# Optimization experiments

Measured on AMD Instinct MI355X. Metric: run time of the kernel, lower is better.

Reference implementation:

```python
import jax, jax.numpy as jnp
import numpy as np

NUM_HEADS = 8
SCALE = 3
TOPKS = [16, 8, 8]  # index 0 = coarsest level


def avg_pool2(t):
    B, C, H, W = t.shape
    return t.reshape(B, C, H // 2, 2, W // 2, 2).mean(axis=(3, 5))


def _to_heads(t, Hi, Wi):
    # [B, C, Hi, Wi] with C = nh*hd (head-major channels) -> [B, nh, Hi*Wi, hd]
    B, C = t.shape[0], t.shape[1]
    hd = C // NUM_HEADS
    return t.reshape(B, NUM_HEADS, hd, Hi * Wi).transpose(0, 1, 3, 2)


def setup_inputs() -> dict:
    key = jax.random.key(0)
    ks = jax.random.split(key, 6)
    B, H, W, C = 2, 96, 96, 128
    N = H * W
    s = 0.02
    return {
        "x": jax.random.normal(ks[0], (B, N, C), jnp.float32),
        "target": jax.random.normal(ks[1], (B, N, C), jnp.float32),
        "Wq": jax.random.normal(ks[2], (C, C), jnp.float32) * s,
        "Wk": jax.random.normal(ks[3], (C, C), jnp.float32) * s,
        "Wv": jax.random.normal(ks[4], (C, C), jnp.float32) * s,
        "Wo": jax.random.normal(ks[5], (C, C), jnp.float32) * s,
        "bo": jnp.zeros((C,), jnp.float32),
        "H": 96,
        "W": 96,
    }


def reference(x, target, Wq, Wk, Wv, Wo, bo, H, W):
    B, N, C = x.shape
    hd = C // NUM_HEADS
    temp = 1.0 / jnp.sqrt(jnp.float32(hd))
    xi = x.transpose(0, 2, 1).reshape(B, C, H, W)
    ti = target.transpose(0, 2, 1).reshape(B, C, H, W)
    # 1x1 conv projections == channel-wise matmul
    q = jnp.einsum('bchw,oc->bohw', xi, Wq)
    k = jnp.einsum('bchw,oc->bohw', ti, Wk)
    v = jnp.einsum('bchw,oc->bohw', ti, Wv)
    qs, ks_, vs, hw = [], [], [], []
    for i in range(SCALE):
        Hi, Wi = H >> i, W >> i
        qs.append(_to_heads(q, Hi, Wi))
        ks_.append(_to_heads(k, Hi, Wi))
        vs.append(_to_heads(v, Hi, Wi))
        hw.append((Hi, Wi))
        if i != SCALE - 1:
            q, k, v = avg_pool2(q), avg_pool2(k), avg_pool2(v)
    # ---- coarsest level: full attention + top-k key selection ----
    i = SCALE - 1
    A = jax.nn.softmax(temp * jnp.einsum('bhnd,bhmd->bhnm', qs[i], ks_[i]), axis=-1)
    msg = jnp.einsum('bhnm,bhmd->bhnd', A, vs[i])  # [B,h,Nc,hd]
    topk_score, topk_idx = jax.lax.top_k(A, TOPKS[0])  # [B,h,Nc,K]
    # ---- refine coarse -> fine over quadtree children of top-k keys ----
    gather = jax.vmap(jax.vmap(lambda arr, idx: arr[idx]))  # over B, h
    for lvl in range(SCALE - 2, -1, -1):
        Hi, Wi = hw[lvl]
        Hp, Wpar = hw[lvl + 1]
        Nf = Hi * Wi
        K = topk_idx.shape[-1]
        yf, xf = jnp.divmod(jnp.arange(Nf), Wi)
        parent = (yf // 2) * Wpar + (xf // 2)  # [Nf] parent query index
        p_idx = topk_idx[:, :, parent, :]  # [B,h,Nf,K] selected coarse keys
        ky, kx = jnp.divmod(p_idx, Wpar)
        dy = jnp.array([0, 0, 1, 1], jnp.int32)
        dx = jnp.array([0, 1, 0, 1], jnp.int32)
        child = ((2 * ky)[..., None] + dy) * Wi + (2 * kx)[..., None] + dx
        cand = child.reshape(B, NUM_HEADS, Nf, K * 4)  # candidate fine keys
        kg = gather(ks_[lvl], cand)  # [B,h,Nf,4K,hd]
        vg = gather(vs[lvl], cand)
        sc = temp * jnp.einsum('bhnd,bhnkd->bhnk', qs[lvl], kg)
        Af = jax.nn.softmax(sc, axis=-1)
        msg_f = jnp.einsum('bhnk,bhnkd->bhnd', Af, vg)
        msg = msg[:, :, parent, :] + msg_f  # assemble with upsampled coarse msg
        if lvl > 0:
            kk = TOPKS[SCALE - 1 - lvl]
            ts, tp = jax.lax.top_k(Af, kk)
            topk_idx = jnp.take_along_axis(cand, tp, axis=-1)
            topk_score = ts
    out = msg.transpose(0, 2, 1, 3).reshape(B, N, C)  # head-major channels
    return out @ Wo.T + bo
```

## Files before the change

kernel.cpp:

```cpp
#include <hip/hip_runtime.h>

#define NB   2
#define NHD  8
#define BH   16
#define HD   16
#define N0   9216
#define N1   2304
#define N2   576
#define W0_  96
#define W1_  48
#define W2_  24
#define M_TOT 18432
#define TEMP 0.25f

__global__ __launch_bounds__(256) void k_proj(const float* __restrict__ x, const float* __restrict__ tg,
    const float* __restrict__ Wq, const float* __restrict__ Wk, const float* __restrict__ Wv,
    float* __restrict__ q0, float* __restrict__ k0, float* __restrict__ v0)
{
    __shared__ __align__(16) float At[16][68];
    __shared__ __align__(16) float Wt[16][132];
    const int t = threadIdx.x;
    const int which = blockIdx.y;
    const float* A  = (which==0)? x : tg;
    const float* Wm = (which==0)? Wq : (which==1? Wk : Wv);
    float* dst      = (which==0)? q0 : (which==1? k0 : v0);
    const int m0 = blockIdx.x * 64;
    const int tx = t & 15, ty = t >> 4;

    float acc[4][8];
#pragma unroll
    for(int i=0;i<4;i++)
#pragma unroll
        for(int j=0;j<8;j++) acc[i][j]=0.f;

    const int ar = t>>2, akq = (t&3)*4;
    const int wo = t>>1, wkq = (t&1)*8;

    for(int kc=0;kc<128;kc+=16){
        float4 av = *(const float4*)(A + (m0+ar)*128 + kc + akq);
        At[akq+0][ar] = av.x;
        At[akq+1][ar] = av.y;
        At[akq+2][ar] = av.z;
        At[akq+3][ar] = av.w;
        float4 w0 = *(const float4*)(Wm + wo*128 + kc + wkq);
        float4 w1 = *(const float4*)(Wm + wo*128 + kc + wkq + 4);
        Wt[wkq+0][wo] = w0.x; Wt[wkq+1][wo] = w0.y;
        Wt[wkq+2][wo] = w0.z; Wt[wkq+3][wo] = w0.w;
        Wt[wkq+4][wo] = w1.x; Wt[wkq+5][wo] = w1.y;
        Wt[wkq+6][wo] = w1.z; Wt[wkq+7][wo] = w1.w;
        __syncthreads();
#pragma unroll
        for(int kk=0;kk<16;kk++){
            float4 a4 = *(const float4*)&At[kk][ty*4];
            float4 wa = *(const float4*)&Wt[kk][tx*4];
            float4 wb = *(const float4*)&Wt[kk][64 + tx*4];
            float avr[4] = {a4.x,a4.y,a4.z,a4.w};
            float wvr[8] = {wa.x,wa.y,wa.z,wa.w, wb.x,wb.y,wb.z,wb.w};
#pragma unroll
            for(int i=0;i<4;i++)
#pragma unroll
                for(int j=0;j<8;j++) acc[i][j] += avr[i]*wvr[j];
        }
        __syncthreads();
    }
    const int hA = tx>>2, dA = (tx&3)*4;
#pragma unroll
    for(int i=0;i<4;i++){
        int m = m0 + ty*4 + i;
        int b = m / N0; int n = m - b*N0;
        float4 sA = make_float4(acc[i][0], acc[i][1], acc[i][2], acc[i][3]);
        float4 sB = make_float4(acc[i][4], acc[i][5], acc[i][6], acc[i][7]);
        *(float4*)(dst + ((b*NHD + hA    )*N0 + n)*16 + dA) = sA;
        *(float4*)(dst + ((b*NHD + hA + 4)*N0 + n)*16 + dA) = sB;
    }
}

__global__ __launch_bounds__(256) void k_pool01(const float4* __restrict__ src0,
    float4* __restrict__ dst1, float4* __restrict__ q2f,
    float4* __restrict__ k2T, float4* __restrict__ v2T)
{
    int tid = blockIdx.x*256 + threadIdx.x;
    if (tid >= 110592) return;
    int d4 = tid & 3;
    int rest = tid >> 2;
    int n2 = rest % N2; int g = rest / N2;
    int yo2 = n2 / W2_, xo2 = n2 - yo2*W2_;

    const float4* s = src0 + g*N0*4;
    float4* d1 = dst1 + g*N1*4;
    float4 l1[4];
#pragma unroll
    for(int yy=0;yy<2;yy++){
#pragma unroll
        for(int xx=0;xx<2;xx++){
            int y1 = 2*yo2+yy, x1 = 2*xo2+xx;
            int n1 = y1*W1_ + x1;
            int cbase = (2*y1)*W0_ + 2*x1;
            float4 a = s[(cbase       )*4 + d4];
            float4 b = s[(cbase+1     )*4 + d4];
            float4 c = s[(cbase+W0_   )*4 + d4];
            float4 d = s[(cbase+W0_+1 )*4 + d4];
            float4 o;
            o.x = 0.25f*(a.x+b.x+c.x+d.x);
            o.y = 0.25f*(a.y+b.y+c.y+d.y);
            o.z = 0.25f*(a.z+b.z+c.z+d.z);
            o.w = 0.25f*(a.w+b.w+c.w+d.w);
            d1[n1*4 + d4] = o;
            l1[yy*2+xx] = o;
        }
    }
    float4 o2;
    o2.x = 0.25f*(l1[0].x+l1[1].x+l1[2].x+l1[3].x);
    o2.y = 0.25f*(l1[0].y+l1[1].y+l1[2].y+l1[3].y);
    o2.z = 0.25f*(l1[0].z+l1[1].z+l1[2].z+l1[3].z);
    o2.w = 0.25f*(l1[0].w+l1[1].w+l1[2].w+l1[3].w);
    int grp = g >> 4, bh = g & 15;
    if (grp == 0)      q2f[(bh*N2 + n2)*4 + d4] = o2;
    else if (grp == 1) k2T[(bh*4 + d4)*N2 + n2] = o2;
    else               v2T[(bh*4 + d4)*N2 + n2] = o2;
}

__device__ __forceinline__ void top16_sel(const float ev[9], int lane, float* cv, int* cx, int* ip)
{
    float head = ev[0];
#pragma unroll
    for(int i=1;i<9;i++) head = fmaxf(head, ev[i]);

    float bv = head;
#pragma unroll
    for(int k=2;k<=64;k<<=1){
#pragma unroll
        for(int j=k>>1;j>=1;j>>=1){
            float pv = __shfl_xor(bv, j);
            bool keepmin = (((lane & k)==0) == ((lane & j)==0));
            bv = keepmin ? fminf(bv,pv) : fmaxf(bv,pv);
        }
    }
    float T = __shfl(bv, 48);

    int ci = 0;
#pragma unroll
    for(int i=0;i<9;i++) ci += (ev[i] >= T) ? 1 : 0;
    int ps = ci;
#pragma unroll
    for(int d=1;d<64;d<<=1){
        int t = __shfl_up(ps, d);
        if (lane >= d) ps += t;
    }
    int excl = ps - ci;
    int C = __shfl(ps, 63);

    int o = excl;
#pragma unroll
    for(int i=0;i<9;i++){
        if (ev[i] >= T){
            cv[o] = ev[i];
            cx[o] = i*64 + lane;
            o++;
        }
    }
    if (lane < 4){ cv[C+lane] = -1.0f; cx[C+lane] = 0x7fffffff; }

    for(int l=lane; l<C; l+=64){
        float mv = cv[l]; int mi = cx[l];
        int rank = 0;
        for(int c=0;c<C;c+=4){
            float4 vv = *(const float4*)(cv + c);
            int4   ii = *(const int4*)(cx + c);
            rank += (vv.x > mv || (vv.x == mv && ii.x < mi)) ? 1 : 0;
            rank += (vv.y > mv || (vv.y == mv && ii.y < mi)) ? 1 : 0;
            rank += (vv.z > mv || (vv.z == mv && ii.z < mi)) ? 1 : 0;
            rank += (vv.w > mv || (vv.w == mv && ii.w < mi)) ? 1 : 0;
        }
        if (rank < 16) ip[rank] = mi;
    }
}

__global__ __launch_bounds__(256) void k_attn2(const float* __restrict__ q2, const float* __restrict__ k2,
    const float* __restrict__ v2, float* __restrict__ msg2, int* __restrict__ idx2)
{
    __shared__ __align__(16) float cval[4][580];
    __shared__ __align__(16) int   cidx[4][580];
    const int bh = blockIdx.x;
    const int wv = threadIdx.x>>6, lane = threadIdx.x&63;
    const int qA = blockIdx.y*8 + wv*2;
    const int qB = qA + 1;

    float qrA[16], qrB[16];
    {
        const float4* qpA = (const float4*)(q2 + (bh*N2 + qA)*16);
        const float4* qpB = (const float4*)(q2 + (bh*N2 + qB)*16);
#pragma unroll
        for(int dq=0;dq<4;dq++){
            float4 va = qpA[dq];
            qrA[dq*4+0]=va.x; qrA[dq*4+1]=va.y; qrA[dq*4+2]=va.z; qrA[dq*4+3]=va.w;
            float4 vb = qpB[dq];
            qrB[dq*4+0]=vb.x; qrB[dq*4+1]=vb.y; qrB[dq*4+2]=vb.z; qrB[dq*4+3]=vb.w;
        }
    }

    const float4* kT = (const float4*)k2 + bh*4*N2;
    const float4* vT = (const float4*)v2 + bh*4*N2;

    float evA[9], evB[9];
    float mxA = -1e30f, mxB = -1e30f;
#pragma unroll
    for(int t9=0;t9<9;t9++){
        int m = t9*64 + lane;
        float sA = 0.f, sB = 0.f;
#pragma unroll
        for(int dg=0;dg<4;dg++){
            float4 kv = kT[dg*N2 + m];
            sA += qrA[dg*4+0]*kv.x + qrA[dg*4+1]*kv.y + qrA[dg*4+2]*kv.z + qrA[dg*4+3]*kv.w;
            sB += qrB[dg*4+0]*kv.x + qrB[dg*4+1]*kv.y + qrB[dg*4+2]*kv.z + qrB[dg*4+3]*kv.w;
        }
        sA *= TEMP; sB *= TEMP;
        evA[t9]=sA; evB[t9]=sB;
        mxA = fmaxf(mxA, sA);
        mxB = fmaxf(mxB, sB);
    }
#pragma unroll
    for(int st=1; st<64; st<<=1){
        mxA = fmaxf(mxA, __shfl_xor(mxA, st));
        mxB = fmaxf(mxB, __shfl_xor(mxB, st));
    }

    float sumA=0.f, sumB=0.f;
    float accA[16], accB[16];
#pragma unroll
    for(int d=0;d<16;d++){ accA[d]=0.f; accB[d]=0.f; }
#pragma unroll
    for(int t9=0;t9<9;t9++){
        int m = t9*64 + lane;
        float eA = expf(evA[t9]-mxA);
        float eB = expf(evB[t9]-mxB);
        evA[t9]=eA; evB[t9]=eB;
        sumA += eA; sumB += eB;
#pragma unroll
        for(int dg=0;dg<4;dg++){
            float4 vv = vT[dg*N2 + m];
            accA[dg*4+0] += eA*vv.x; accA[dg*4+1] += eA*vv.y;
            accA[dg*4+2] += eA*vv.z; accA[dg*4+3] += eA*vv.w;
            accB[dg*4+0] += eB*vv.x; accB[dg*4+1] += eB*vv.y;
            accB[dg*4+2] += eB*vv.z; accB[dg*4+3] += eB*vv.w;
        }
    }
#pragma unroll
    for(int st=1; st<64; st<<=1){
        sumA += __shfl_xor(sumA, st);
        sumB += __shfl_xor(sumB, st);
    }

    const bool b5 = (lane & 32) != 0;
    const bool b4 = (lane & 16) != 0;
    const bool b3 = (lane & 8) != 0;
    const bool b2 = (lane & 4) != 0;
#pragma unroll
    for(int which=0; which<2; which++){
        float* acc = which ? accB : accA;
        float sum  = which ? sumB : sumA;
        int   q    = which ? qB   : qA;
        float r8[8];
#pragma unroll
        for(int i=0;i<8;i++){
            float snd  = b5 ? acc[i]   : acc[i+8];
            float kept = b5 ? acc[i+8] : acc[i];
            r8[i] = kept + __shfl_xor(snd, 32);
        }
        float r4[4];
#pragma unroll
        for(int i=0;i<4;i++){
            float snd  = b4 ? r8[i]   : r8[i+4];
            float kept = b4 ? r8[i+4] : r8[i];
            r4[i] = kept + __shfl_xor(snd, 16);
        }
        float r2[2];
#pragma unroll
        for(int i=0;i<2;i++){
            float snd  = b3 ? r4[i]   : r4[i+2];
            float kept = b3 ? r4[i+2] : r4[i];
            r2[i] = kept + __shfl_xor(snd, 8);
        }
        {
            float snd  = b2 ? r2[0] : r2[1];
            float kept = b2 ? r2[1] : r2[0];
            r2[0] = kept + __shfl_xor(snd, 4);
        }
        r2[0] += __shfl_xor(r2[0], 2);
        r2[0] += __shfl_xor(r2[0], 1);
        float inv = 1.0f/sum;
        if ((lane&3)==0){
            msg2[(bh*N2+q)*16 + (lane>>2)] = r2[0]*inv;
        }
    }

    top16_sel(evA, lane, cval[wv], cidx[wv], idx2 + (bh*N2+qA)*16);
    top16_sel(evB, lane, cval[wv], cidx[wv], idx2 + (bh*N2+qB)*16);
}

__global__ __launch_bounds__(256) void k_ref10(
    const float* __restrict__ q1, const float* __restrict__ k1, const float* __restrict__ v1,
    const float* __restrict__ q0, const float* __restrict__ k0, const float* __restrict__ v0,
    const float* __restrict__ msg2, const int* __restrict__ idx2, float* __restrict__ msg0)
{
    __shared__ float msg1s[4][16];
    __shared__ int   idx1s[4][8];
    const int bid = (blockIdx.x & 7)*1152 + (blockIdx.x >> 3);
    const int bh = bid / 576, tile = bid - bh*576;
    const int tyy = tile / 24, txx = tile - tyy*24;
    const int py0 = tyy*2, px0 = txx*2;
    const int wv = threadIdx.x>>6, lane = threadIdx.x&63;

    const int ppy = py0 + (wv>>1), ppx = px0 + (wv&1);

    {
        const int n  = ppy*W1_ + ppx;
        const int par = (ppy>>1)*W2_ + (ppx>>1);
        const int kk = lane>>2, tt = lane&3, dy = tt>>1, dx = tt&1;
        int p = idx2[(bh*N2+par)*16 + kk];
        int ky = p / W2_, kx = p - ky*W2_;
        int child = (2*ky+dy)*W1_ + 2*kx+dx;

        const float* qp = q1 + (bh*N1+n)*16;
        float qr[16];
#pragma unroll
        for(int d=0; d<16; d+=4){
            float4 qq = *(const float4*)(qp+d);
            qr[d]=qq.x; qr[d+1]=qq.y; qr[d+2]=qq.z; qr[d+3]=qq.w;
        }
        const float4* kp = (const float4*)(k1 + (bh*N1+child)*16);
        float s = 0.f;
#pragma unroll
        for(int dq=0;dq<4;dq++){
            float4 kv = kp[dq];
            s += qr[dq*4+0]*kv.x + qr[dq*4+1]*kv.y + qr[dq*4+2]*kv.z + qr[dq*4+3]*kv.w;
        }
        s *= TEMP;
        float e = expf(s);
        float sum = e;
#pragma unroll
        for(int st=1; st<64; st<<=1) sum += __shfl_xor(sum, st);

        float acc[16];
        const float4* vp = (const float4*)(v1 + (bh*N1+child)*16);
#pragma unroll
        for(int dq=0;dq<4;dq++){
            float4 vv = vp[dq];
            acc[dq*4+0]=e*vv.x; acc[dq*4+1]=e*vv.y; acc[dq*4+2]=e*vv.z; acc[dq*4+3]=e*vv.w;
        }
        const bool b5 = (lane & 32) != 0;
        float r8[8];
#pragma unroll
        for(int ii=0;ii<8;ii++){
            float snd  = b5 ? acc[ii]   : acc[ii+8];
            float kept = b5 ? acc[ii+8] : acc[ii];
            r8[ii] = kept + __shfl_xor(snd, 32);
        }
        const bool b4 = (lane & 16) != 0;
        float r4[4];
#pragma unroll
        for(int ii=0;ii<4;ii++){
            float snd  = b4 ? r8[ii]   : r8[ii+4];
            float kept = b4 ? r8[ii+4] : r8[ii];
            r4[ii] = kept + __shfl_xor(snd, 16);
        }
        const bool b3 = (lane & 8) != 0;
        float r2[2];
#pragma unroll
        for(int ii=0;ii<2;ii++){
            float snd  = b3 ? r4[ii]   : r4[ii+2];
            float kept = b3 ? r4[ii+2] : r4[ii];
            r2[ii] = kept + __shfl_xor(snd, 8);
        }
        const bool b2 = (lane & 4) != 0;
        {
            float snd  = b2 ? r2[0] : r2[1];
            float kept = b2 ? r2[1] : r2[0];
            r2[0] = kept + __shfl_xor(snd, 4);
        }
        r2[0] += __shfl_xor(r2[0], 2);
        r2[0] += __shfl_xor(r2[0], 1);

        float inv1 = 1.0f/sum;
        if ((lane&3)==0){
            int d = lane>>2;
            msg1s[wv][d] = msg2[(bh*N2+par)*16 + d] + r2[0]*inv1;
        }

        float bv = s;
#pragma unroll
        for(int kb=2;kb<=64;kb<<=1){
#pragma unroll
            for(int jb=kb>>1;jb>=1;jb>>=1){
                float pv = __shfl_xor(bv, jb);
                bool keepmin = (((lane & kb)==0) == ((lane & jb)==0));
                bv = keepmin ? fminf(bv,pv) : fmaxf(bv,pv);
            }
        }
        float T8 = __shfl(bv, 56);
        unsigned long long mgt = __ballot(s > T8);
        unsigned long long meq = __ballot(s == T8);
        int ngt = (int)__popcll(mgt);
        int ltg = __builtin_amdgcn_mbcnt_lo((unsigned)mgt, 0);
        ltg = __builtin_amdgcn_mbcnt_hi((unsigned)(mgt>>32), ltg);
        int lte = __builtin_amdgcn_mbcnt_lo((unsigned)meq, 0);
        lte = __builtin_amdgcn_mbcnt_hi((unsigned)(meq>>32), lte);
        int slot = (s > T8) ? ltg : ((s == T8) ? (ngt + lte) : 8);
        if (slot < 8) idx1s[wv][slot] = child;
    }

    const int j = lane & 31, sub = lane >> 5;
    const int kk = j>>2, tt = j&3, dy = tt>>1, dx = tt&1;
    int p = idx1s[wv][kk];
    int ky = p / W1_, kx = p - ky*W1_;
    int child = (2*ky+dy)*W0_ + 2*kx+dx;

    float kr[16];
    {
        const float4* kp = (const float4*)(k0 + (bh*N0+child)*16);
#pragma unroll
        for(int dq=0;dq<4;dq++){
            float4 kv = kp[dq];
            kr[dq*4+0]=kv.x; kr[dq*4+1]=kv.y; kr[dq*4+2]=kv.z; kr[dq*4+3]=kv.w;
        }
    }
    const int cy0 = 2*ppy, cx0 = 2*ppx + sub;
    int nq[2];
    float s_[2];
#pragma unroll
    for(int it=0; it<2; it++){
        nq[it] = (cy0+it)*W0_ + cx0;
        const float* qp = q0 + (bh*N0+nq[it])*16;
        float qr[16];
#pragma unroll
        for(int d=0; d<16; d+=4){
            float4 qq = *(const float4*)(qp+d);
            qr[d]=qq.x; qr[d+1]=qq.y; qr[d+2]=qq.z; qr[d+3]=qq.w;
        }
        float s = 0.f;
#pragma unroll
        for(int dq=0;dq<4;dq++){
            s += qr[dq*4+0]*kr[dq*4+0] + qr[dq*4+1]*kr[dq*4+1]
               + qr[dq*4+2]*kr[dq*4+2] + qr[dq*4+3]*kr[dq*4+3];
        }
        s_[it] = s * TEMP;
    }
    float vr[16];
    {
        const float4* vp = (const float4*)(v0 + (bh*N0+child)*16);
#pragma unroll
        for(int dq=0;dq<4;dq++){
            float4 vv = vp[dq];
            vr[dq*4+0]=vv.x; vr[dq*4+1]=vv.y; vr[dq*4+2]=vv.z; vr[dq*4+3]=vv.w;
        }
    }
    const float m1d = msg1s[wv][j>>1];

#pragma unroll
    for(int it=0; it<2; it++){
        float e = expf(s_[it]);
        float sum = e;
#pragma unroll
        for(int st=1; st<32; st<<=1) sum += __shfl_xor(sum, st);

        float acc[16];
#pragma unroll
        for(int d=0;d<16;d++) acc[d] = e*vr[d];

        const bool b4 = (j & 16) != 0;
        float r8[8];
#pragma unroll
        for(int ii=0;ii<8;ii++){
            float snd  = b4 ? acc[ii]   : acc[ii+8];
            float kept = b4 ? acc[ii+8] : acc[ii];
            r8[ii] = kept + __shfl_xor(snd, 16);
        }
        const bool b3 = (j & 8) != 0;
        float r4[4];
#pragma unroll
        for(int ii=0;ii<4;ii++){
            float snd  = b3 ? r8[ii]   : r8[ii+4];
            float kept = b3 ? r8[ii+4] : r8[ii];
            r4[ii] = kept + __shfl_xor(snd, 8);
        }
        const bool b2 = (j & 4) != 0;
        float r2[2];
#pragma unroll
        for(int ii=0;ii<2;ii++){
            float snd  = b2 ? r4[ii]   : r4[ii+2];
            float kept = b2 ? r4[ii+2] : r4[ii];
            r2[ii] = kept + __shfl_xor(snd, 4);
        }
        const bool b1 = (j & 2) != 0;
        {
            float snd  = b1 ? r2[0] : r2[1];
            float kept = b1 ? r2[1] : r2[0];
            r2[0] = kept + __shfl_xor(snd, 2);
        }
        r2[0] += __shfl_xor(r2[0], 1);

        float inv = 1.0f/sum;
        if ((j&1)==0){
            int d = j>>1;
            int b_ = bh>>3, h = bh&7;
            msg0[(b_*N0+nq[it])*128 + h*16 + d] = m1d + r2[0]*inv;
        }
    }
}

__global__ __launch_bounds__(256) void k_out(const float* __restrict__ msg0, const float* __restrict__ Wo,
    const float* __restrict__ bo, float* __restrict__ out)
{
    __shared__ __align__(16) float At[16][68];
    __shared__ __align__(16) float Wt[16][132];
    const int t = threadIdx.x;
    const int m0 = blockIdx.x * 64;
    const int tx = t & 15, ty = t >> 4;

    float acc[4][8];
#pragma unroll
    for(int i=0;i<4;i++)
#pragma unroll
        for(int j=0;j<8;j++) acc[i][j]=0.f;

    const int ar = t>>2, akq = (t&3)*4;
    const int wo = t>>1, wkq = (t&1)*8;

    for(int kc=0;kc<128;kc+=16){
        float4 av = *(const float4*)(msg0 + (m0+ar)*128 + kc + akq);
        At[akq+0][ar] = av.x;
        At[akq+1][ar] = av.y;
        At[akq+2][ar] = av.z;
        At[akq+3][ar] = av.w;
        float4 w0 = *(const float4*)(Wo + wo*128 + kc + wkq);
        float4 w1 = *(const float4*)(Wo + wo*128 + kc + wkq + 4);
        Wt[wkq+0][wo] = w0.x; Wt[wkq+1][wo] = w0.y;
        Wt[wkq+2][wo] = w0.z; Wt[wkq+3][wo] = w0.w;
        Wt[wkq+4][wo] = w1.x; Wt[wkq+5][wo] = w1.y;
        Wt[wkq+6][wo] = w1.z; Wt[wkq+7][wo] = w1.w;
        __syncthreads();
#pragma unroll
        for(int kk=0;kk<16;kk++){
            float4 a4 = *(const float4*)&At[kk][ty*4];
            float4 wa = *(const float4*)&Wt[kk][tx*4];
            float4 wb = *(const float4*)&Wt[kk][64 + tx*4];
            float avr[4] = {a4.x,a4.y,a4.z,a4.w};
            float wvr[8] = {wa.x,wa.y,wa.z,wa.w, wb.x,wb.y,wb.z,wb.w};
#pragma unroll
            for(int i=0;i<4;i++)
#pragma unroll
                for(int j=0;j<8;j++) acc[i][j] += avr[i]*wvr[j];
        }
        __syncthreads();
    }
#pragma unroll
    for(int i=0;i<4;i++){
        int m = m0 + ty*4 + i;
        float4 sA = make_float4(acc[i][0]+bo[tx*4+0], acc[i][1]+bo[tx*4+1],
                                acc[i][2]+bo[tx*4+2], acc[i][3]+bo[tx*4+3]);
        float4 sB = make_float4(acc[i][4]+bo[64+tx*4+0], acc[i][5]+bo[64+tx*4+1],
                                acc[i][6]+bo[64+tx*4+2], acc[i][7]+bo[64+tx*4+3]);
        *(float4*)(out + m*128 + tx*4)      = sA;
        *(float4*)(out + m*128 + 64 + tx*4) = sB;
    }
}

extern "C" void kernel_launch(void* const* d_in, const int* in_sizes, int n_in,
                              void* d_out, int out_size, void* d_ws, size_t ws_size,
                              hipStream_t stream) {
    const float* x  = (const float*)d_in[0];
    const float* tg = (const float*)d_in[1];
    const float* Wq = (const float*)d_in[2];
    const float* Wk = (const float*)d_in[3];
    const float* Wv = (const float*)d_in[4];
    const float* Wo = (const float*)d_in[5];
    const float* bo = (const float*)d_in[6];

    float* ws = (float*)d_ws;
    float* q0   = ws + 0;
    float* k0   = ws + 2359296;
    float* v0   = ws + 4718592;
    float* q1   = ws + 7077888;
    float* k1   = ws + 7667712;
    float* v1   = ws + 8257536;
    float* q2   = ws + 8847360;
    float* k2   = ws + 8994816;
    float* v2   = ws + 9142272;
    float* msg2 = ws + 9289728;
    float* msg0 = ws + 10027008;
    int*   idx2 = (int*)(ws + 12386304);

    k_proj<<<dim3(288,3), 256, 0, stream>>>(x, tg, Wq, Wk, Wv, q0, k0, v0);
    k_pool01<<<432, 256, 0, stream>>>((const float4*)q0, (float4*)q1,
                                      (float4*)q2, (float4*)k2, (float4*)v2);
    k_attn2<<<dim3(16,72), 256, 0, stream>>>(q2, k2, v2, msg2, idx2);
    k_ref10<<<9216, 256, 0, stream>>>(q1, k1, v1, q0, k0, v0, msg2, idx2, msg0);
    k_out<<<288, 256, 0, stream>>>(msg0, Wo, bo, (float*)d_out);
}
```

Before: 206.7 us.

## Double-buffer K/V loads in coarse attention and widen refine tile per block

In the coarse attention kernel, K and V loads are software-pipelined with two register buffers so the next chunk's loads are issued before the current chunk's math. The refine kernel now has each wave handle two level-1 parents and each thread four level-0 queries, so the block count is halved and each loaded fine key/value is reused across four queries instead of two. This cuts redundant gathers and block launch overhead at the cost of more registers per thread and fewer blocks in flight.

```diff
diff --git a/kernel.cpp b/kernel.cpp
--- a/kernel.cpp
+++ b/kernel.cpp
@@ -176,6 +176,26 @@
     }
 }
 
+#define LOADK(KB, T9) { int m_=(T9)*64+lane; \
+    KB[0]=kT[0*N2+m_]; KB[1]=kT[1*N2+m_]; KB[2]=kT[2*N2+m_]; KB[3]=kT[3*N2+m_]; }
+#define LOADV(VB, T9) { int m_=(T9)*64+lane; \
+    VB[0]=vT[0*N2+m_]; VB[1]=vT[1*N2+m_]; VB[2]=vT[2*N2+m_]; VB[3]=vT[3*N2+m_]; }
+#define STEPK(T9, KB) { float sA=0.f, sB=0.f; \
+    _Pragma("unroll") \
+    for(int dg=0;dg<4;dg++){ float4 kv=KB[dg]; \
+      sA += qrA[dg*4+0]*kv.x + qrA[dg*4+1]*kv.y + qrA[dg*4+2]*kv.z + qrA[dg*4+3]*kv.w; \
+      sB += qrB[dg*4+0]*kv.x + qrB[dg*4+1]*kv.y + qrB[dg*4+2]*kv.z + qrB[dg*4+3]*kv.w; } \
+    sA *= TEMP; sB *= TEMP; \
+    evA[T9]=sA; evB[T9]=sB; \
+    mxA = fmaxf(mxA, sA); mxB = fmaxf(mxB, sB); }
+#define STEPV(T9, VB) { \
+    float eA=expf(evA[T9]-mxA), eB=expf(evB[T9]-mxB); \
+    evA[T9]=eA; evB[T9]=eB; sumA+=eA; sumB+=eB; \
+    _Pragma("unroll") \
+    for(int dg=0;dg<4;dg++){ float4 vv=VB[dg]; \
+      accA[dg*4+0]+=eA*vv.x; accA[dg*4+1]+=eA*vv.y; accA[dg*4+2]+=eA*vv.z; accA[dg*4+3]+=eA*vv.w; \
+      accB[dg*4+0]+=eB*vv.x; accB[dg*4+1]+=eB*vv.y; accB[dg*4+2]+=eB*vv.z; accB[dg*4+3]+=eB*vv.w; } }
+
 __global__ __launch_bounds__(256) void k_attn2(const float* __restrict__ q2, const float* __restrict__ k2,
     const float* __restrict__ v2, float* __restrict__ msg2, int* __restrict__ idx2)
 {
@@ -204,20 +224,17 @@
 
     float evA[9], evB[9];
     float mxA = -1e30f, mxB = -1e30f;
-#pragma unroll
-    for(int t9=0;t9<9;t9++){
-        int m = t9*64 + lane;
-        float sA = 0.f, sB = 0.f;
-#pragma unroll
-        for(int dg=0;dg<4;dg++){
-            float4 kv = kT[dg*N2 + m];
-            sA += qrA[dg*4+0]*kv.x + qrA[dg*4+1]*kv.y + qrA[dg*4+2]*kv.z + qrA[dg*4+3]*kv.w;
-            sB += qrB[dg*4+0]*kv.x + qrB[dg*4+1]*kv.y + qrB[dg*4+2]*kv.z + qrB[dg*4+3]*kv.w;
-        }
-        sA *= TEMP; sB *= TEMP;
-        evA[t9]=sA; evB[t9]=sB;
-        mxA = fmaxf(mxA, sA);
-        mxB = fmaxf(mxB, sB);
+    {
+        float4 ka[4], kb[4];
+        LOADK(ka, 0);
+#pragma unroll
+        for(int t2=0;t2<4;t2++){
+            LOADK(kb, 2*t2+1);
+            STEPK(2*t2, ka);
+            LOADK(ka, 2*t2+2);
+            STEPK(2*t2+1, kb);
+        }
+        STEPK(8, ka);
     }
 #pragma unroll
     for(int st=1; st<64; st<<=1){
@@ -229,21 +246,17 @@
     float accA[16], accB[16];
 #pragma unroll
     for(int d=0;d<16;d++){ accA[d]=0.f; accB[d]=0.f; }
-#pragma unroll
-    for(int t9=0;t9<9;t9++){
-        int m = t9*64 + lane;
-        float eA = expf(evA[t9]-mxA);
-        float eB = expf(evB[t9]-mxB);
-        evA[t9]=eA; evB[t9]=eB;
-        sumA += eA; sumB += eB;
-#pragma unroll
-        for(int dg=0;dg<4;dg++){
-            float4 vv = vT[dg*N2 + m];
-            accA[dg*4+0] += eA*vv.x; accA[dg*4+1] += eA*vv.y;
-            accA[dg*4+2] += eA*vv.z; accA[dg*4+3] += eA*vv.w;
-            accB[dg*4+0] += eB*vv.x; accB[dg*4+1] += eB*vv.y;
-            accB[dg*4+2] += eB*vv.z; accB[dg*4+3] += eB*vv.w;
-        }
+    {
+        float4 va_[4], vb[4];
+        LOADV(va_, 0);
+#pragma unroll
+        for(int t2=0;t2<4;t2++){
+            LOADV(vb, 2*t2+1);
+            STEPV(2*t2, va_);
+            LOADV(va_, 2*t2+2);
+            STEPV(2*t2+1, vb);
+        }
+        STEPV(8, va_);
     }
 #pragma unroll
     for(int st=1; st<64; st<<=1){
@@ -303,17 +316,20 @@
     const float* __restrict__ q0, const float* __restrict__ k0, const float* __restrict__ v0,
     const float* __restrict__ msg2, const int* __restrict__ idx2, float* __restrict__ msg0)
 {
-    __shared__ float msg1s[4][16];
-    __shared__ int   idx1s[4][8];
-    const int bid = (blockIdx.x & 7)*1152 + (blockIdx.x >> 3);
-    const int bh = bid / 576, tile = bid - bh*576;
-    const int tyy = tile / 24, txx = tile - tyy*24;
-    const int py0 = tyy*2, px0 = txx*2;
+    __shared__ float msg1s[8][16];
+    __shared__ int   idx1s[8][8];
+    const int bid = (blockIdx.x & 7)*576 + (blockIdx.x >> 3);
+    const int bh = bid / 288, tile = bid - bh*288;
+    const int tyy = tile / 12, txx = tile - tyy*12;
+    const int py0 = tyy*2, px0 = txx*4;
     const int wv = threadIdx.x>>6, lane = threadIdx.x&63;
 
-    const int ppy = py0 + (wv>>1), ppx = px0 + (wv&1);
-
-    {
+    const int ppy  = py0 + (wv>>1);
+    const int ppx0 = px0 + (wv&1)*2;
+
+#pragma unroll
+    for(int pp=0; pp<2; pp++){
+        const int ppx = ppx0 + pp;
         const int n  = ppy*W1_ + ppx;
         const int par = (ppy>>1)*W2_ + (ppx>>1);
         const int kk = lane>>2, tt = lane&3, dy = tt>>1, dx = tt&1;
@@ -384,16 +400,16 @@
         float inv1 = 1.0f/sum;
         if ((lane&3)==0){
             int d = lane>>2;
-            msg1s[wv][d] = msg2[(bh*N2+par)*16 + d] + r2[0]*inv1;
+            msg1s[wv*2+pp][d] = msg2[(bh*N2+par)*16 + d] + r2[0]*inv1;
         }
 
         float bv = s;
 #pragma unroll
-        for(int kb=2;kb<=64;kb<<=1){
-#pragma unroll
-            for(int jb=kb>>1;jb>=1;jb>>=1){
+        for(int kb2=2;kb2<=64;kb2<<=1){
+#pragma unroll
+            for(int jb=kb2>>1;jb>=1;jb>>=1){
                 float pv = __shfl_xor(bv, jb);
-                bool keepmin = (((lane & kb)==0) == ((lane & jb)==0));
+                bool keepmin = (((lane & kb2)==0) == ((lane & jb)==0));
                 bv = keepmin ? fminf(bv,pv) : fmaxf(bv,pv);
             }
         }
@@ -406,12 +422,14 @@
         int lte = __builtin_amdgcn_mbcnt_lo((unsigned)meq, 0);
         lte = __builtin_amdgcn_mbcnt_hi((unsigned)(meq>>32), lte);
         int slot = (s > T8) ? ltg : ((s == T8) ? (ngt + lte) : 8);
-        if (slot < 8) idx1s[wv][slot] = child;
-    }
-
-    const int j = lane & 31, sub = lane >> 5;
+        if (slot < 8) idx1s[wv*2+pp][slot] = child;
+    }
+
+    const int sub = lane>>5, j = lane&31;
+    const int ppx = ppx0 + sub;
+    const int slot = wv*2 + sub;
     const int kk = j>>2, tt = j&3, dy = tt>>1, dx = tt&1;
-    int p = idx1s[wv][kk];
+    int p = idx1s[slot][kk];
     int ky = p / W1_, kx = p - ky*W1_;
     int child = (2*ky+dy)*W0_ + 2*kx+dx;
 
@@ -424,12 +442,12 @@
             kr[dq*4+0]=kv.x; kr[dq*4+1]=kv.y; kr[dq*4+2]=kv.z; kr[dq*4+3]=kv.w;
         }
     }
-    const int cy0 = 2*ppy, cx0 = 2*ppx + sub;
-    int nq[2];
-    float s_[2];
-#pragma unroll
-    for(int it=0; it<2; it++){
-        nq[it] = (cy0+it)*W0_ + cx0;
+    const int cy0 = 2*ppy, cx0 = 2*ppx;
+    int nq[4];
+    float s_[4];
+#pragma unroll
+    for(int it=0; it<4; it++){
+        nq[it] = (cy0+(it>>1))*W0_ + cx0 + (it&1);
         const float* qp = q0 + (bh*N0+nq[it])*16;
         float qr[16];
 #pragma unroll
@@ -454,10 +472,10 @@
             vr[dq*4+0]=vv.x; vr[dq*4+1]=vv.y; vr[dq*4+2]=vv.z; vr[dq*4+3]=vv.w;
         }
     }
-    const float m1d = msg1s[wv][j>>1];
-
-#pragma unroll
-    for(int it=0; it<2; it++){
+    const float m1d = msg1s[slot][j>>1];
+
+#pragma unroll
+    for(int it=0; it<4; it++){
         float e = expf(s_[it]);
         float sum = e;
 #pragma unroll
@@ -594,6 +612,6 @@
     k_pool01<<<432, 256, 0, stream>>>((const float4*)q0, (float4*)q1,
                                       (float4*)q2, (float4*)k2, (float4*)v2);
     k_attn2<<<dim3(16,72), 256, 0, stream>>>(q2, k2, v2, msg2, idx2);
-    k_ref10<<<9216, 256, 0, stream>>>(q1, k1, v1, q0, k0, v0, msg2, idx2, msg0);
+    k_ref10<<<4608, 256, 0, stream>>>(q1, k1, v1, q0, k0, v0, msg2, idx2, msg0);
     k_out<<<288, 256, 0, stream>>>(msg0, Wo, bo, (float*)d_out);
 }
```

After: 211.6 us. 2.4% more time.
